# Kernel tuning notes

Measured on AMD Instinct MI355X. Metric: run time of the kernel, lower is better.

The kernel has to match this reference:

```python
import jax, jax.numpy as jnp
import numpy as np

B, T, D, H = 2, 2048, 1024, 16
HD = D // H            # 64
FH = 2752              # SwiGLU hidden: round64(int(2*4*D/3))
BETA_INIT = 0.5


def rmsnorm(x, w, eps=1e-6):
    x32 = x.astype(jnp.float32)
    r = jax.lax.rsqrt(jnp.mean(x32 * x32, axis=-1, keepdims=True) + eps)
    return (x32 * r).astype(x.dtype) * w


def rope(x, cos, sin):
    # x: (B,H,T,HD); cos/sin: (T,HD//2)
    d2 = x.shape[-1] // 2
    x1, x2 = x[..., :d2], x[..., d2:]
    return jnp.concatenate([x1 * cos - x2 * sin, x2 * cos + x1 * sin], axis=-1)


def delta_res(x, h, gn_w, g_w, g_b, wv_w, eps_k=1e-6):
    # k-hat = normalize(h); k = k_hat / sqrt(d)
    h32 = h.astype(jnp.float32)
    nrm = jnp.sqrt(jnp.sum(h32 * h32, axis=-1, keepdims=True))
    k = (h32 / jnp.maximum(nrm, eps_k)).astype(x.dtype) * (1.0 / np.sqrt(D))
    c = rmsnorm(x, gn_w)
    logit = c @ g_w + g_b                                   # (B,T)
    beta = (2.0 * jax.nn.sigmoid(logit.astype(jnp.float32))).astype(x.dtype)[..., None]
    v = jax.nn.sigmoid(x @ wv_w)[..., None]                 # (B,T,1)
    kTx = jnp.sum(k * x, axis=-1, keepdims=True)
    return x + beta * (v - kTx) * k


def setup_inputs() -> dict:
    key = jax.random.key(0)
    ks = jax.random.split(key, 12)
    s = 0.02
    gb = np.float32(np.log(BETA_INIT / 2.0 / (1.0 - BETA_INIT / 2.0 + 1e-8)))
    return {
        "x": jax.random.normal(ks[0], (B, T, D), jnp.float32),
        "wq": jax.random.normal(ks[1], (D, D), jnp.float32) * s,
        "wk": jax.random.normal(ks[2], (D, D), jnp.float32) * s,
        "wv": jax.random.normal(ks[3], (D, D), jnp.float32) * s,
        "wo": jax.random.normal(ks[4], (D, D), jnp.float32) * s,
        "qn_w": jnp.ones((HD,), jnp.float32),
        "kn_w": jnp.ones((HD,), jnp.float32),
        "attn_norm_w": jnp.ones((D,), jnp.float32),
        "g1_norm_w": jnp.ones((D,), jnp.float32),
        "g1_w": jax.random.normal(ks[5], (D,), jnp.float32) * s,
        "g1_b": jnp.asarray(gb),
        "wv1": jax.random.normal(ks[6], (D,), jnp.float32) * s,
        "mlp_norm_w": jnp.ones((D,), jnp.float32),
        "w1": jax.random.normal(ks[7], (FH, D), jnp.float32) * s,
        "w2": jax.random.normal(ks[8], (D, FH), jnp.float32) * s,
        "w3": jax.random.normal(ks[9], (FH, D), jnp.float32) * s,
        "g2_norm_w": jnp.ones((D,), jnp.float32),
        "g2_w": jax.random.normal(ks[10], (D,), jnp.float32) * s,
        "g2_b": jnp.asarray(gb),
        "wv2": jax.random.normal(ks[11], (D,), jnp.float32) * s,
    }


def reference(x, wq, wk, wv, wo, qn_w, kn_w, attn_norm_w,
              g1_norm_w, g1_w, g1_b, wv1, mlp_norm_w, w1, w2, w3,
              g2_norm_w, g2_w, g2_b, wv2):
    # ---- attention sublayer (pre-norm) ----
    xc = rmsnorm(x, attn_norm_w)
    q = (xc @ wq.T).reshape(B, T, H, HD).swapaxes(1, 2)   # (B,H,T,HD)
    k = (xc @ wk.T).reshape(B, T, H, HD).swapaxes(1, 2)
    v = (xc @ wv.T).reshape(B, T, H, HD).swapaxes(1, 2)
    q = rmsnorm(q, qn_w)
    k = rmsnorm(k, kn_w)
    inv_freq = 1.0 / (10000.0 ** (jnp.arange(0, HD, 2, dtype=jnp.float32) / HD))
    freqs = jnp.arange(T, dtype=jnp.float32)[:, None] * inv_freq[None, :]  # (T,HD/2)
    cos, sin = jnp.cos(freqs), jnp.sin(freqs)
    q = rope(q, cos, sin)
    k = rope(k, cos, sin)
    scale = 1.0 / np.sqrt(HD)
    scores = jnp.einsum('bhqd,bhkd->bhqk', q, k) * scale
    causal = jnp.where(jnp.arange(T)[:, None] >= jnp.arange(T)[None, :], 0.0, -jnp.inf).astype(scores.dtype)
    attn = jax.nn.softmax(scores + causal, axis=-1)
    out = jnp.einsum('bhqk,bhkd->bhqd', attn, v)
    h_attn = out.swapaxes(1, 2).reshape(B, T, D) @ wo.T
    x = delta_res(x, h_attn, g1_norm_w, g1_w, g1_b, wv1)
    # ---- MLP sublayer (pre-norm SwiGLU) ----
    xm = rmsnorm(x, mlp_norm_w)
    h_mlp = (jax.nn.silu(xm @ w1.T) * (xm @ w3.T)) @ w2.T
    x = delta_res(x, h_mlp, g2_norm_w, g2_w, g2_b, wv2)
    return x
```

## Files before the change

kernel.cpp:

```cpp
#include <hip/hip_runtime.h>
#include <hip/hip_bf16.h>
#include <math.h>

using bf16 = __hip_bfloat16;
typedef __bf16 bf16x8 __attribute__((ext_vector_type(8)));
typedef float f32x4 __attribute__((ext_vector_type(4)));

static constexpr int B_ = 2, T_ = 2048, D_ = 1024, H_ = 16, HD_ = 64, FH_ = 2752;
static constexpr int BT = B_ * T_;

struct __align__(8)  bh4 { bf16 h[4]; };
struct __align__(16) bh8 { bf16 h[8]; };

#define DEV static __device__ __forceinline__

DEV float b2f(bf16 v) { return __bfloat162float(v); }
DEV bf16  f2b(float v) { return __float2bfloat16(v); }
DEV __bf16 f2bb(float f) { __hip_bfloat16 h = __float2bfloat16(f); return *reinterpret_cast<__bf16*>(&h); }
DEV float sigmoidf_(float x) { return 1.0f / (1.0f + __expf(-x)); }

DEV void load4f(const bf16* p, float* v) {
    bh4 t = *reinterpret_cast<const bh4*>(p);
#pragma unroll
    for (int i = 0; i < 4; ++i) v[i] = b2f(t.h[i]);
}
DEV void load4f(const float* p, float* v) {
    float4 t = *reinterpret_cast<const float4*>(p);
    v[0] = t.x; v[1] = t.y; v[2] = t.z; v[3] = t.w;
}
DEV void store4(float* p, const float* v) {
    float4 t; t.x = v[0]; t.y = v[1]; t.z = v[2]; t.w = v[3];
    *reinterpret_cast<float4*>(p) = t;
}
DEV float waveReduceSum(float v) {
#pragma unroll
    for (int m = 32; m; m >>= 1) v += __shfl_xor(v, m);
    return v;
}

DEV void gl_lds16(const bf16* g, bf16* lds_base) {
    __builtin_amdgcn_global_load_lds(
        (const __attribute__((address_space(1))) void*)g,
        (__attribute__((address_space(3))) void*)lds_base, 16, 0, 0);
}

__global__ __launch_bounds__(256) void k_rope_tables(float* __restrict__ cost, float* __restrict__ sint) {
    int idx = blockIdx.x * 256 + threadIdx.x;
    if (idx >= T_ * 32) return;
    int t = idx >> 5, j = idx & 31;
    float inv = powf(10000.0f, -(float)j * (1.0f / 32.0f));
    float f = (float)t * inv;
    cost[idx] = cosf(f);
    sint[idx] = sinf(f);
}

__global__ __launch_bounds__(256) void k_f2b(const float* __restrict__ in, bf16* __restrict__ out, int n8) {
    int i = blockIdx.x * 256 + threadIdx.x;
    if (i >= n8) return;
    const float4* p = reinterpret_cast<const float4*>(in + (size_t)i * 8);
    float4 a = p[0], b = p[1];
    bh8 o;
    o.h[0] = f2b(a.x); o.h[1] = f2b(a.y); o.h[2] = f2b(a.z); o.h[3] = f2b(a.w);
    o.h[4] = f2b(b.x); o.h[5] = f2b(b.y); o.h[6] = f2b(b.z); o.h[7] = f2b(b.w);
    *reinterpret_cast<bh8*>(out + (size_t)i * 8) = o;
}

__global__ __launch_bounds__(256) void k_f2b_pair(const float* __restrict__ w1, const float* __restrict__ w3,
                                                  bf16* __restrict__ outp, int n8tot) {
    int i = blockIdx.x * 256 + threadIdx.x;
    if (i >= n8tot) return;
    int r = i >> 7, c8 = i & 127;
    int sel = (r >> 4) & 1;
    int j = ((r >> 5) << 4) | (r & 15);
    const float* src = (sel ? w3 : w1) + (size_t)j * D_ + c8 * 8;
    float4 a = reinterpret_cast<const float4*>(src)[0];
    float4 b = reinterpret_cast<const float4*>(src)[1];
    bh8 o;
    o.h[0] = f2b(a.x); o.h[1] = f2b(a.y); o.h[2] = f2b(a.z); o.h[3] = f2b(a.w);
    o.h[4] = f2b(b.x); o.h[5] = f2b(b.y); o.h[6] = f2b(b.z); o.h[7] = f2b(b.w);
    *reinterpret_cast<bh8*>(outp + (size_t)r * D_ + c8 * 8) = o;
}

__global__ __launch_bounds__(256) void k_rmsnorm(const float* __restrict__ x, const float* __restrict__ w,
                                                 bf16* __restrict__ out) {
    int row = blockIdx.x, tid = threadIdx.x;
    const float* xr = x + (size_t)row * D_;
    int base = tid * 4;
    float v[4];
    load4f(xr + base, v);
    float ss = v[0]*v[0] + v[1]*v[1] + v[2]*v[2] + v[3]*v[3];
    ss = waveReduceSum(ss);
    __shared__ float red[4];
    if ((tid & 63) == 0) red[tid >> 6] = ss;
    __syncthreads();
    ss = red[0] + red[1] + red[2] + red[3];
    float r = rsqrtf(ss * (1.0f / D_) + 1e-6f);
    float wv[4];
    load4f(w + base, wv);
    bh4 o;
#pragma unroll
    for (int i = 0; i < 4; ++i) o.h[i] = f2b(v[i] * r * wv[i]);
    *reinterpret_cast<bh4*>(out + (size_t)row * D_ + base) = o;
}

template <int EPI>
__global__ __launch_bounds__(512) void k_gemm256(const bf16* __restrict__ A, const bf16* __restrict__ W,
                                                 bf16* __restrict__ C, int M, int N, int K) {
    __shared__ bf16 sA[2][256 * 32];
    __shared__ bf16 sB[2][128 * 32];
    int tid = threadIdx.x, lane = tid & 63, wid = tid >> 6;
    int m0 = blockIdx.x * 256, n0 = blockIdx.y * 128;
    int wr = wid >> 1, wc = wid & 1;
    int l16 = lane & 15, lg = lane >> 4;
    int srow = lane >> 2;
    int scol = ((lane & 3) ^ ((lane >> 3) & 3)) * 8;
    int rchunk = (lg ^ ((l16 >> 1) & 3)) * 8;

    f32x4 acc[4][4] = {};

#define STAGE(buf, k0)                                                                   \
    {                                                                                    \
        _Pragma("unroll")                                                                \
        for (int c = 0; c < 2; ++c) {                                                    \
            int r0 = wid * 32 + c * 16;                                                  \
            gl_lds16(&A[(size_t)(m0 + r0 + srow) * K + (k0) + scol], &sA[buf][r0 * 32]); \
        }                                                                                \
        {                                                                                \
            int r0 = wid * 16;                                                           \
            gl_lds16(&W[(size_t)(n0 + r0 + srow) * K + (k0) + scol], &sB[buf][r0 * 32]); \
        }                                                                                \
    }

    int nk = K >> 5;
    STAGE(0, 0);
    if (nk > 1) STAGE(1, 32);
    for (int t = 0; t < nk; ++t) {
        if (t + 1 < nk) { asm volatile("s_waitcnt vmcnt(3)" ::: "memory"); }
        else            { asm volatile("s_waitcnt vmcnt(0)" ::: "memory"); }
        __builtin_amdgcn_s_barrier();
        __builtin_amdgcn_sched_barrier(0);
        int cur = t & 1;
        bf16x8 af[4], bfr[4];
#pragma unroll
        for (int m = 0; m < 4; ++m)
            af[m] = *reinterpret_cast<const bf16x8*>(&sA[cur][(wr * 64 + m * 16 + l16) * 32 + rchunk]);
#pragma unroll
        for (int n = 0; n < 4; ++n)
            bfr[n] = *reinterpret_cast<const bf16x8*>(&sB[cur][(wc * 64 + n * 16 + l16) * 32 + rchunk]);
#pragma unroll
        for (int m = 0; m < 4; ++m)
#pragma unroll
            for (int n = 0; n < 4; ++n)
                acc[m][n] = __builtin_amdgcn_mfma_f32_16x16x32_bf16(af[m], bfr[n], acc[m][n], 0, 0, 0);
        __builtin_amdgcn_sched_barrier(0);
        __builtin_amdgcn_s_barrier();
        if (t + 2 < nk) STAGE(cur, (t + 2) * 32);
    }
#undef STAGE

    int rbase = m0 + wr * 64;
    if (EPI == 1) {
        int Ng = N >> 1;
        int gbase = (n0 >> 1) + wc * 32;
#pragma unroll
        for (int m = 0; m < 4; ++m) {
#pragma unroll
            for (int n2 = 0; n2 < 2; ++n2) {
                int gcol = gbase + n2 * 16 + l16;
#pragma unroll
                for (int r = 0; r < 4; ++r) {
                    int row = rbase + m * 16 + lg * 4 + r;
                    float a1 = acc[m][n2 * 2][r];
                    float a3 = acc[m][n2 * 2 + 1][r];
                    C[(size_t)row * Ng + gcol] = f2b(a1 * sigmoidf_(a1) * a3);
                }
            }
        }
    } else {
        int cbase = n0 + wc * 64;
#pragma unroll
        for (int m = 0; m < 4; ++m) {
#pragma unroll
            for (int n = 0; n < 4; ++n) {
                int col = cbase + n * 16 + l16;
#pragma unroll
                for (int r = 0; r < 4; ++r) {
                    int row = rbase + m * 16 + lg * 4 + r;
                    C[(size_t)row * N + col] = f2b(acc[m][n][r]);
                }
            }
        }
    }
}

__global__ __launch_bounds__(256) void k_gemm64(const bf16* __restrict__ A, const bf16* __restrict__ W,
                                                bf16* __restrict__ C, int M, int N, int K) {
    __shared__ bf16 sA[2][128 * 32];
    __shared__ bf16 sB[2][64 * 32];
    int tid = threadIdx.x, lane = tid & 63, wid = tid >> 6;
    int m0 = blockIdx.x * 128, n0 = blockIdx.y * 64;
    int wr = wid;
    int l16 = lane & 15, lg = lane >> 4;
    int srow = lane >> 2;
    int scol = ((lane & 3) ^ ((lane >> 3) & 3)) * 8;
    int rchunk = (lg ^ ((l16 >> 1) & 3)) * 8;

    f32x4 acc[2][4] = {};

#define STAGE(buf, k0)                                                                   \
    {                                                                                    \
        _Pragma("unroll")                                                                \
        for (int c = 0; c < 2; ++c) {                                                    \
            int r0 = wid * 32 + c * 16;                                                  \
            gl_lds16(&A[(size_t)(m0 + r0 + srow) * K + (k0) + scol], &sA[buf][r0 * 32]); \
        }                                                                                \
        {                                                                                \
            int r0 = wid * 16;                                                           \
            gl_lds16(&W[(size_t)(n0 + r0 + srow) * K + (k0) + scol], &sB[buf][r0 * 32]); \
        }                                                                                \
    }

    int nk = K >> 5;
    STAGE(0, 0);
    if (nk > 1) STAGE(1, 32);
    for (int t = 0; t < nk; ++t) {
        if (t + 1 < nk) { asm volatile("s_waitcnt vmcnt(3)" ::: "memory"); }
        else            { asm volatile("s_waitcnt vmcnt(0)" ::: "memory"); }
        __builtin_amdgcn_s_barrier();
        __builtin_amdgcn_sched_barrier(0);
        int cur = t & 1;
        bf16x8 af[2], bfr[4];
#pragma unroll
        for (int m = 0; m < 2; ++m)
            af[m] = *reinterpret_cast<const bf16x8*>(&sA[cur][(wr * 32 + m * 16 + l16) * 32 + rchunk]);
#pragma unroll
        for (int n = 0; n < 4; ++n)
            bfr[n] = *reinterpret_cast<const bf16x8*>(&sB[cur][(n * 16 + l16) * 32 + rchunk]);
#pragma unroll
        for (int m = 0; m < 2; ++m)
#pragma unroll
            for (int n = 0; n < 4; ++n)
                acc[m][n] = __builtin_amdgcn_mfma_f32_16x16x32_bf16(af[m], bfr[n], acc[m][n], 0, 0, 0);
        __builtin_amdgcn_sched_barrier(0);
        __builtin_amdgcn_s_barrier();
        if (t + 2 < nk) STAGE(cur, (t + 2) * 32);
    }
#undef STAGE

    int rbase = m0 + wr * 32;
#pragma unroll
    for (int m = 0; m < 2; ++m) {
#pragma unroll
        for (int n = 0; n < 4; ++n) {
            int col = n0 + n * 16 + l16;
#pragma unroll
            for (int r = 0; r < 4; ++r) {
                int row = rbase + m * 16 + lg * 4 + r;
                C[(size_t)row * N + col] = f2b(acc[m][n][r]);
            }
        }
    }
}

__global__ __launch_bounds__(256) void k_qk_norm_rope(const bf16* __restrict__ qin, const float* __restrict__ wn,
                                                      const float* __restrict__ cost, const float* __restrict__ sint,
                                                      bf16* __restrict__ qout, float scale, int ld, int off) {
    int tid = threadIdx.x;
    int g = blockIdx.x * 4 + (tid >> 6);
    int d = tid & 63;
    int h = g % H_, t = (g / H_) % T_, b = g / (H_ * T_);
    float v = b2f(qin[(size_t)(b * T_ + t) * ld + off + h * HD_ + d]);
    float ss = waveReduceSum(v * v);
    float r = rsqrtf(ss * (1.0f / HD_) + 1e-6f);
    float xn = v * r * wn[d];
    float p = __shfl_xor(xn, 32);
    float c = cost[t * 32 + (d & 31)], s = sint[t * 32 + (d & 31)];
    float o = (d < 32) ? (xn * c - p * s) : (xn * c + p * s);
    qout[((size_t)(b * H_ + h) * T_ + t) * HD_ + d] = f2b(o * scale);
}

__global__ __launch_bounds__(256) void k_v_transpose(const bf16* __restrict__ vin, bf16* __restrict__ vt,
                                                     int ld, int off) {
    __shared__ bf16 tile[64][72];
    int tid = threadIdx.x;
    int bh = blockIdx.y;
    int t0 = blockIdx.x * 64;
    int b = bh >> 4, h = bh & 15;
#pragma unroll
    for (int i = 0; i < 16; ++i) {
        int lin = i * 256 + tid;
        int tl = lin >> 6, d = lin & 63;
        tile[tl][d] = vin[(size_t)(b * T_ + t0 + tl) * ld + off + h * HD_ + d];
    }
    __syncthreads();
#pragma unroll
    for (int i = 0; i < 16; ++i) {
        int lin = i * 256 + tid;
        int d = lin >> 6, tl = lin & 63;
        vt[((size_t)bh * HD_ + d) * T_ + t0 + tl] = tile[tl][d];
    }
}

template <bool MASKED>
DEV void fa3_tile(const bf16* __restrict__ kl, const bf16* __restrict__ vl,
                  int l16, int lg, int qloc,
                  const bf16x8 qf0, const bf16x8 qf1,
                  f32x4* acc, float& m_r, float& l_r) {
    f32x4 s[8];
#pragma unroll
    for (int n = 0; n < 8; ++n) {
        int kv = n * 16 + l16;
        bf16x8 kf0 = *reinterpret_cast<const bf16x8*>(&kl[kv * 64 + (((lg ^ kv) & 7) << 3)]);
        bf16x8 kf1 = *reinterpret_cast<const bf16x8*>(&kl[kv * 64 + ((((4 + lg) ^ kv) & 7) << 3)]);
        f32x4 t = {};
        t = __builtin_amdgcn_mfma_f32_16x16x32_bf16(kf0, qf0, t, 0, 0, 0);
        t = __builtin_amdgcn_mfma_f32_16x16x32_bf16(kf1, qf1, t, 0, 0, 0);
        s[n] = t;
    }
    if (MASKED) {
#pragma unroll
        for (int n = 0; n < 8; ++n)
#pragma unroll
            for (int r = 0; r < 4; ++r)
                if (n * 16 + lg * 4 + r > qloc) s[n][r] = -INFINITY;
    }
    float mx = -INFINITY;
#pragma unroll
    for (int n = 0; n < 8; ++n)
#pragma unroll
        for (int r = 0; r < 4; ++r) mx = fmaxf(mx, s[n][r]);
    mx = fmaxf(mx, __shfl_xor(mx, 16));
    mx = fmaxf(mx, __shfl_xor(mx, 32));
    float mnew = fmaxf(m_r, mx);
    float corr = __expf(m_r - mnew);
    m_r = mnew;
    float ps = 0.0f;
#pragma unroll
    for (int n = 0; n < 8; ++n)
#pragma unroll
        for (int r = 0; r < 4; ++r) {
            float e = __expf(s[n][r] - mnew);
            s[n][r] = e;
            ps += e;
        }
    l_r = l_r * corr + ps;
#pragma unroll
    for (int np = 0; np < 4; ++np) acc[np] = acc[np] * corr;

    bf16x8 pb[4];
#pragma unroll
    for (int n2 = 0; n2 < 4; ++n2)
#pragma unroll
        for (int j = 0; j < 8; ++j)
            pb[n2][j] = f2bb(s[2 * n2 + (j >> 2)][j & 3]);

    int d15 = l16;
    int eoff = (lg & 1) * 4;
#pragma unroll
    for (int n2 = 0; n2 < 4; ++n2) {
        int c0 = (n2 * 4 + (lg >> 1));
        int c1 = c0 + 2;
#pragma unroll
        for (int np = 0; np < 4; ++np) {
            int d = np * 16 + l16;
            union { bf16x8 v; bh4 q[2]; } u;
            u.q[0] = *reinterpret_cast<const bh4*>(&vl[d * 128 + ((c0 ^ d15) << 3) + eoff]);
            u.q[1] = *reinterpret_cast<const bh4*>(&vl[d * 128 + ((c1 ^ d15) << 3) + eoff]);
            acc[np] = __builtin_amdgcn_mfma_f32_16x16x32_bf16(u.v, pb[n2], acc[np], 0, 0, 0);
        }
    }
}

__global__ __launch_bounds__(256) void k_flash(const bf16* __restrict__ Q, const bf16* __restrict__ Kk,
                                               const bf16* __restrict__ Vt, bf16* __restrict__ Out) {
    __shared__ bf16 kl[128 * 64];
    __shared__ bf16 vl[64 * 128];
    int tid = threadIdx.x, lane = tid & 63, w = tid >> 6;
    int l16 = lane & 15, lg = lane >> 4;
    int L = blockIdx.x;
    int xcd = L & 7, m = L >> 3;
    int bh = xcd * 4 + (m & 3);
    int qi = (T_ / 128 - 1) - (m >> 2);
    int q0 = qi * 128;
    int b = bh >> 4, h = bh & 15;
    const bf16* qb = Q + (size_t)bh * T_ * HD_;
    const bf16* kb = Kk + (size_t)bh * T_ * HD_;
    const bf16* vb = Vt + (size_t)bh * HD_ * T_;

    bf16x8 qfr[2][2];
#pragma unroll
    for (int f = 0; f < 2; ++f) {
        int qrow = q0 + w * 32 + f * 16 + l16;
        const bf16* qp = qb + (size_t)qrow * HD_ + lg * 8;
        qfr[f][0] = *reinterpret_cast<const bf16x8*>(qp);
        qfr[f][1] = *reinterpret_cast<const bf16x8*>(qp + 32);
    }
    f32x4 acc[2][4] = {};
    float m_r[2] = {-INFINITY, -INFINITY};
    float l_r[2] = {0.0f, 0.0f};

    for (int kv0 = 0; kv0 <= q0; kv0 += 128) {
        __syncthreads();
#pragma unroll
        for (int i = 0; i < 4; ++i) {
            int idx = i * 256 + tid;
            int kv = idx >> 3, c = idx & 7;
            *reinterpret_cast<bh8*>(&kl[kv * 64 + (((c ^ kv) & 7) << 3)]) =
                *reinterpret_cast<const bh8*>(&kb[(size_t)(kv0 + kv) * HD_ + c * 8]);
        }
#pragma unroll
        for (int i = 0; i < 4; ++i) {
            int idx = i * 256 + tid;
            int d = idx >> 4, c = idx & 15;
            *reinterpret_cast<bh8*>(&vl[d * 128 + (((c ^ d) & 15) << 3)]) =
                *reinterpret_cast<const bh8*>(&vb[(size_t)d * T_ + kv0 + c * 8]);
        }
        __syncthreads();
        if (kv0 == q0) {
#pragma unroll
            for (int f = 0; f < 2; ++f)
                fa3_tile<true>(kl, vl, l16, lg, w * 32 + f * 16 + l16,
                               qfr[f][0], qfr[f][1], acc[f], m_r[f], l_r[f]);
        } else {
#pragma unroll
            for (int f = 0; f < 2; ++f)
                fa3_tile<false>(kl, vl, l16, lg, 0,
                                qfr[f][0], qfr[f][1], acc[f], m_r[f], l_r[f]);
        }
    }
#pragma unroll
    for (int f = 0; f < 2; ++f) {
        float lt = l_r[f];
        lt += __shfl_xor(lt, 16);
        lt += __shfl_xor(lt, 32);
        float inv = 1.0f / lt;
        int qrow = q0 + w * 32 + f * 16 + l16;
#pragma unroll
        for (int np = 0; np < 4; ++np) {
            bh4 o;
#pragma unroll
            for (int r = 0; r < 4; ++r) o.h[r] = f2b(acc[f][np][r] * inv);
            *reinterpret_cast<bh4*>(&Out[(size_t)(b * T_ + qrow) * D_ + h * HD_ + np * 16 + lg * 4]) = o;
        }
    }
}

template <int WRITE_XM>
__global__ __launch_bounds__(256) void k_delta_res(const float* __restrict__ x, const bf16* __restrict__ h,
                                                   const float* __restrict__ gn_w, const float* __restrict__ g_w,
                                                   const float* __restrict__ g_b, const float* __restrict__ wv_w,
                                                   float* __restrict__ out,
                                                   bf16* __restrict__ xm_out, const float* __restrict__ mlp_w) {
    int row = blockIdx.x, tid = threadIdx.x;
    int base = tid * 4;
    float xv[4], hv[4], gnv[4], gwv[4], wvv[4];
    load4f(x + (size_t)row * D_ + base, xv);
    load4f(h + (size_t)row * D_ + base, hv);
    load4f(gn_w + base, gnv);
    load4f(g_w + base, gwv);
    load4f(wv_w + base, wvv);
    float s_h2 = 0, s_x2 = 0, s_xg = 0, s_xv = 0, s_hx = 0;
#pragma unroll
    for (int i = 0; i < 4; ++i) {
        s_h2 += hv[i] * hv[i];
        s_x2 += xv[i] * xv[i];
        s_xg += xv[i] * gnv[i] * gwv[i];
        s_xv += xv[i] * wvv[i];
        s_hx += hv[i] * xv[i];
    }
    s_h2 = waveReduceSum(s_h2); s_x2 = waveReduceSum(s_x2); s_xg = waveReduceSum(s_xg);
    s_xv = waveReduceSum(s_xv); s_hx = waveReduceSum(s_hx);
    __shared__ float red[4][5];
    int wid = tid >> 6;
    if ((tid & 63) == 0) {
        red[wid][0] = s_h2; red[wid][1] = s_x2; red[wid][2] = s_xg;
        red[wid][3] = s_xv; red[wid][4] = s_hx;
    }
    __syncthreads();
    s_h2 = red[0][0] + red[1][0] + red[2][0] + red[3][0];
    s_x2 = red[0][1] + red[1][1] + red[2][1] + red[3][1];
    s_xg = red[0][2] + red[1][2] + red[2][2] + red[3][2];
    s_xv = red[0][3] + red[1][3] + red[2][3] + red[3][3];
    s_hx = red[0][4] + red[1][4] + red[2][4] + red[3][4];

    float r = rsqrtf(s_x2 * (1.0f / D_) + 1e-6f);
    float logit = r * s_xg + g_b[0];
    float beta = 2.0f * sigmoidf_(logit);
    float vsig = sigmoidf_(s_xv);
    float nrm = sqrtf(s_h2);
    float ks = (1.0f / 32.0f) / fmaxf(nrm, 1e-6f);
    float coef = beta * (vsig - ks * s_hx) * ks;
    float o[4];
#pragma unroll
    for (int i = 0; i < 4; ++i) o[i] = xv[i] + coef * hv[i];
    store4(out + (size_t)row * D_ + base, o);

    if (WRITE_XM) {
        float s2 = o[0]*o[0] + o[1]*o[1] + o[2]*o[2] + o[3]*o[3];
        s2 = waveReduceSum(s2);
        __shared__ float red2[4];
        __syncthreads();
        if ((tid & 63) == 0) red2[wid] = s2;
        __syncthreads();
        s2 = red2[0] + red2[1] + red2[2] + red2[3];
        float rr = rsqrtf(s2 * (1.0f / D_) + 1e-6f);
        float mw[4];
        load4f(mlp_w + base, mw);
        bh4 ob;
#pragma unroll
        for (int i = 0; i < 4; ++i) ob.h[i] = f2b(o[i] * rr * mw[i]);
        *reinterpret_cast<bh4*>(xm_out + (size_t)row * D_ + base) = ob;
    }
}

extern "C" void kernel_launch(void* const* d_in, const int* in_sizes, int n_in,
                              void* d_out, int out_size, void* d_ws, size_t ws_size,
                              hipStream_t stream) {
    const float* x       = (const float*)d_in[0];
    const float* wq      = (const float*)d_in[1];
    const float* wk      = (const float*)d_in[2];
    const float* wv      = (const float*)d_in[3];
    const float* wo      = (const float*)d_in[4];
    const float* qn_w    = (const float*)d_in[5];
    const float* kn_w    = (const float*)d_in[6];
    const float* attn_nw = (const float*)d_in[7];
    const float* g1_nw   = (const float*)d_in[8];
    const float* g1_w    = (const float*)d_in[9];
    const float* g1_b    = (const float*)d_in[10];
    const float* wv1     = (const float*)d_in[11];
    const float* mlp_nw  = (const float*)d_in[12];
    const float* w1      = (const float*)d_in[13];
    const float* w2      = (const float*)d_in[14];
    const float* w3      = (const float*)d_in[15];
    const float* g2_nw   = (const float*)d_in[16];
    const float* g2_w    = (const float*)d_in[17];
    const float* g2_b    = (const float*)d_in[18];
    const float* wv2     = (const float*)d_in[19];
    float* out = (float*)d_out;

    char* ws = (char*)d_ws;
    const size_t KB = 1024;
    const size_t MB = 1024 * 1024;
    float* cost = (float*)(ws);
    float* sint = (float*)(ws + 256 * KB);
    bf16* XC = (bf16*)(ws + 512 * KB);
    bf16* Bb = (bf16*)(ws + 512 * KB + 8  * MB);
    bf16* Cb = (bf16*)(ws + 512 * KB + 16 * MB);
    bf16* Db = (bf16*)(ws + 512 * KB + 24 * MB);
    bf16* Eb = (bf16*)(ws + 512 * KB + 32 * MB);
    bf16* Fb = (bf16*)(ws + 512 * KB + 40 * MB);
    bf16* Gb = (bf16*)(ws + 512 * KB + 48 * MB);
    float* x1 = (float*)(ws + 512 * KB + 56 * MB);

    bf16* wqkv = Eb;
    bf16* qkv  = Bb;
    bf16* wbo  = XC;
    bf16* attn_out = Bb;
    bf16* wpair = Bb;
    bf16* w2b  = Db;
    bf16* g    = Eb;
    bf16* hmlp = XC;

    const int nDD = D_ * D_ / 8, nFD = FH_ * D_ / 8;
    dim3 blk(256);

    k_rope_tables<<<dim3((T_ * 32) / 256), blk, 0, stream>>>(cost, sint);

    k_rmsnorm<<<dim3(BT), blk, 0, stream>>>(x, attn_nw, XC);
    k_f2b<<<dim3((nDD + 255) / 256), blk, 0, stream>>>(wq, wqkv, nDD);
    k_f2b<<<dim3((nDD + 255) / 256), blk, 0, stream>>>(wk, wqkv + (size_t)D_ * D_, nDD);
    k_f2b<<<dim3((nDD + 255) / 256), blk, 0, stream>>>(wv, wqkv + (size_t)2 * D_ * D_, nDD);

    k_gemm256<0><<<dim3(16, 24), dim3(512), 0, stream>>>(XC, wqkv, qkv, BT, 3 * D_, D_);

    k_qk_norm_rope<<<dim3(BT * H_ / 4), blk, 0, stream>>>(qkv, qn_w, cost, sint, Eb, 0.125f, 3 * D_, 0);
    k_qk_norm_rope<<<dim3(BT * H_ / 4), blk, 0, stream>>>(qkv, kn_w, cost, sint, Fb, 1.0f, 3 * D_, D_);
    k_v_transpose<<<dim3(T_ / 64, B_ * H_), blk, 0, stream>>>(qkv, Gb, 3 * D_, 2 * D_);

    k_f2b<<<dim3((nDD + 255) / 256), blk, 0, stream>>>(wo, wbo, nDD);
    k_flash<<<dim3((T_ / 128) * B_ * H_), blk, 0, stream>>>(Eb, Fb, Gb, attn_out);

    k_gemm64<<<dim3(32, 16), blk, 0, stream>>>(attn_out, wbo, Cb, BT, D_, D_);

    k_delta_res<1><<<dim3(BT), blk, 0, stream>>>(x, Cb, g1_nw, g1_w, g1_b, wv1, x1, XC, mlp_nw);

    k_f2b_pair<<<dim3((2 * nFD + 255) / 256), blk, 0, stream>>>(w1, w3, wpair, 2 * nFD);
    k_f2b<<<dim3((nFD + 255) / 256), blk, 0, stream>>>(w2, w2b, nFD);

    k_gemm256<1><<<dim3(16, 43), dim3(512), 0, stream>>>(XC, wpair, g, BT, 2 * FH_, D_);

    k_gemm64<<<dim3(32, 16), blk, 0, stream>>>(g, w2b, hmlp, BT, D_, FH_);

    k_delta_res<0><<<dim3(BT), blk, 0, stream>>>(x1, hmlp, g2_nw, g2_w, g2_b, wv2, out, nullptr, nullptr);
}
```

Before: 282.9 us.

## Load GEMM A-fragments directly from global into registers, dropping A shared-memory staging

Both GEMM kernels stop staging the A tile through LDS. Each wave now loads its own A fragments straight from global memory into registers, double-buffered in two register sets, and only the shared W tile still goes through LDS. The loop is unrolled by two with adjusted vmcnt waits. This removes LDS traffic and LDS capacity for A, which could allow higher occupancy. The cost is more registers, uncoalesced per-row global loads, and duplicate A reads across the two column waves. Launch-bounds occupancy hints are also added to the GEMM and flash kernels.

```diff
diff --git a/kernel.cpp b/kernel.cpp
--- a/kernel.cpp
+++ b/kernel.cpp
@@ -104,9 +104,8 @@
 }
 
 template <int EPI>
-__global__ __launch_bounds__(512) void k_gemm256(const bf16* __restrict__ A, const bf16* __restrict__ W,
-                                                 bf16* __restrict__ C, int M, int N, int K) {
-    __shared__ bf16 sA[2][256 * 32];
+__global__ __launch_bounds__(512, 3) void k_gemm256(const bf16* __restrict__ A, const bf16* __restrict__ W,
+                                                    bf16* __restrict__ C, int M, int N, int K) {
     __shared__ bf16 sB[2][128 * 32];
     int tid = threadIdx.x, lane = tid & 63, wid = tid >> 6;
     int m0 = blockIdx.x * 256, n0 = blockIdx.y * 128;
@@ -116,47 +115,58 @@
     int scol = ((lane & 3) ^ ((lane >> 3) & 3)) * 8;
     int rchunk = (lg ^ ((l16 >> 1) & 3)) * 8;
 
+    const bf16* Ab = A + (size_t)(m0 + wr * 64 + l16) * K + lg * 8;
+
     f32x4 acc[4][4] = {};
-
-#define STAGE(buf, k0)                                                                   \
+    bf16x8 afA[4], afB[4];
+
+#define STB(buf, k0)                                                                     \
+    {                                                                                    \
+        int r0 = wid * 16;                                                               \
+        gl_lds16(&W[(size_t)(n0 + r0 + srow) * K + (k0) + scol], &sB[buf][r0 * 32]);     \
+    }
+#define GLA(dst, k0)                                                                     \
     {                                                                                    \
         _Pragma("unroll")                                                                \
-        for (int c = 0; c < 2; ++c) {                                                    \
-            int r0 = wid * 32 + c * 16;                                                  \
-            gl_lds16(&A[(size_t)(m0 + r0 + srow) * K + (k0) + scol], &sA[buf][r0 * 32]); \
-        }                                                                                \
-        {                                                                                \
-            int r0 = wid * 16;                                                           \
-            gl_lds16(&W[(size_t)(n0 + r0 + srow) * K + (k0) + scol], &sB[buf][r0 * 32]); \
-        }                                                                                \
+        for (int m = 0; m < 4; ++m)                                                      \
+            dst[m] = *reinterpret_cast<const bf16x8*>(Ab + (size_t)m * 16 * K + (k0));   \
+    }
+#define COMPUTE(buf, af)                                                                 \
+    {                                                                                    \
+        bf16x8 bfr[4];                                                                   \
+        _Pragma("unroll")                                                                \
+        for (int n = 0; n < 4; ++n)                                                      \
+            bfr[n] = *reinterpret_cast<const bf16x8*>(&sB[buf][(wc * 64 + n * 16 + l16) * 32 + rchunk]); \
+        _Pragma("unroll")                                                                \
+        for (int m = 0; m < 4; ++m)                                                      \
+            _Pragma("unroll")                                                            \
+            for (int n = 0; n < 4; ++n)                                                  \
+                acc[m][n] = __builtin_amdgcn_mfma_f32_16x16x32_bf16(af[m], bfr[n], acc[m][n], 0, 0, 0); \
     }
 
     int nk = K >> 5;
-    STAGE(0, 0);
-    if (nk > 1) STAGE(1, 32);
-    for (int t = 0; t < nk; ++t) {
-        if (t + 1 < nk) { asm volatile("s_waitcnt vmcnt(3)" ::: "memory"); }
+    STB(0, 0); GLA(afA, 0);
+    STB(1, 32); GLA(afB, 32);
+    for (int t = 0; t < nk; t += 2) {
+        asm volatile("s_waitcnt vmcnt(5)" ::: "memory");
+        __builtin_amdgcn_s_barrier();
+        __builtin_amdgcn_sched_barrier(0);
+        COMPUTE(0, afA);
+        __builtin_amdgcn_sched_barrier(0);
+        __builtin_amdgcn_s_barrier();
+        if (t + 2 < nk) { STB(0, (t + 2) * 32); GLA(afA, (t + 2) * 32); }
+        if (t + 2 < nk) { asm volatile("s_waitcnt vmcnt(5)" ::: "memory"); }
         else            { asm volatile("s_waitcnt vmcnt(0)" ::: "memory"); }
         __builtin_amdgcn_s_barrier();
         __builtin_amdgcn_sched_barrier(0);
-        int cur = t & 1;
-        bf16x8 af[4], bfr[4];
-#pragma unroll
-        for (int m = 0; m < 4; ++m)
-            af[m] = *reinterpret_cast<const bf16x8*>(&sA[cur][(wr * 64 + m * 16 + l16) * 32 + rchunk]);
-#pragma unroll
-        for (int n = 0; n < 4; ++n)
-            bfr[n] = *reinterpret_cast<const bf16x8*>(&sB[cur][(wc * 64 + n * 16 + l16) * 32 + rchunk]);
-#pragma unroll
-        for (int m = 0; m < 4; ++m)
-#pragma unroll
-            for (int n = 0; n < 4; ++n)
-                acc[m][n] = __builtin_amdgcn_mfma_f32_16x16x32_bf16(af[m], bfr[n], acc[m][n], 0, 0, 0);
-        __builtin_amdgcn_sched_barrier(0);
-        __builtin_amdgcn_s_barrier();
-        if (t + 2 < nk) STAGE(cur, (t + 2) * 32);
-    }
-#undef STAGE
+        COMPUTE(1, afB);
+        __builtin_amdgcn_sched_barrier(0);
+        __builtin_amdgcn_s_barrier();
+        if (t + 3 < nk) { STB(1, (t + 3) * 32); GLA(afB, (t + 3) * 32); }
+    }
+#undef STB
+#undef GLA
+#undef COMPUTE
 
     int rbase = m0 + wr * 64;
     if (EPI == 1) {
@@ -193,61 +203,70 @@
     }
 }
 
-__global__ __launch_bounds__(256) void k_gemm64(const bf16* __restrict__ A, const bf16* __restrict__ W,
-                                                bf16* __restrict__ C, int M, int N, int K) {
-    __shared__ bf16 sA[2][128 * 32];
+__global__ __launch_bounds__(256, 4) void k_gemm64(const bf16* __restrict__ A, const bf16* __restrict__ W,
+                                                   bf16* __restrict__ C, int M, int N, int K) {
     __shared__ bf16 sB[2][64 * 32];
     int tid = threadIdx.x, lane = tid & 63, wid = tid >> 6;
     int m0 = blockIdx.x * 128, n0 = blockIdx.y * 64;
-    int wr = wid;
     int l16 = lane & 15, lg = lane >> 4;
     int srow = lane >> 2;
     int scol = ((lane & 3) ^ ((lane >> 3) & 3)) * 8;
     int rchunk = (lg ^ ((l16 >> 1) & 3)) * 8;
 
+    const bf16* Ab = A + (size_t)(m0 + wid * 32 + l16) * K + lg * 8;
+
     f32x4 acc[2][4] = {};
-
-#define STAGE(buf, k0)                                                                   \
+    bf16x8 afA[2], afB[2];
+
+#define STB(buf, k0)                                                                     \
+    {                                                                                    \
+        int r0 = wid * 16;                                                               \
+        gl_lds16(&W[(size_t)(n0 + r0 + srow) * K + (k0) + scol], &sB[buf][r0 * 32]);     \
+    }
+#define GLA(dst, k0)                                                                     \
     {                                                                                    \
         _Pragma("unroll")                                                                \
-        for (int c = 0; c < 2; ++c) {                                                    \
-            int r0 = wid * 32 + c * 16;                                                  \
-            gl_lds16(&A[(size_t)(m0 + r0 + srow) * K + (k0) + scol], &sA[buf][r0 * 32]); \
-        }                                                                                \
-        {                                                                                \
-            int r0 = wid * 16;                                                           \
-            gl_lds16(&W[(size_t)(n0 + r0 + srow) * K + (k0) + scol], &sB[buf][r0 * 32]); \
-        }                                                                                \
+        for (int m = 0; m < 2; ++m)                                                      \
+            dst[m] = *reinterpret_cast<const bf16x8*>(Ab + (size_t)m * 16 * K + (k0));   \
+    }
+#define COMPUTE(buf, af)                                                                 \
+    {                                                                                    \
+        bf16x8 bfr[4];                                                                   \
+        _Pragma("unroll")                                                                \
+        for (int n = 0; n < 4; ++n)                                                      \
+            bfr[n] = *reinterpret_cast<const bf16x8*>(&sB[buf][(n * 16 + l16) * 32 + rchunk]); \
+        _Pragma("unroll")                                                                \
+        for (int m = 0; m < 2; ++m)                                                      \
+            _Pragma("unroll")                                                            \
+            for (int n = 0; n < 4; ++n)                                                  \
+                acc[m][n] = __builtin_amdgcn_mfma_f32_16x16x32_bf16(af[m], bfr[n], acc[m][n], 0, 0, 0); \
     }
 
     int nk = K >> 5;
-    STAGE(0, 0);
-    if (nk > 1) STAGE(1, 32);
-    for (int t = 0; t < nk; ++t) {
-        if (t + 1 < nk) { asm volatile("s_waitcnt vmcnt(3)" ::: "memory"); }
+    STB(0, 0); GLA(afA, 0);
+    STB(1, 32); GLA(afB, 32);
+    for (int t = 0; t < nk; t += 2) {
+        asm volatile("s_waitcnt vmcnt(3)" ::: "memory");
+        __builtin_amdgcn_s_barrier();
+        __builtin_amdgcn_sched_barrier(0);
+        COMPUTE(0, afA);
+        __builtin_amdgcn_sched_barrier(0);
+        __builtin_amdgcn_s_barrier();
+        if (t + 2 < nk) { STB(0, (t + 2) * 32); GLA(afA, (t + 2) * 32); }
+        if (t + 2 < nk) { asm volatile("s_waitcnt vmcnt(3)" ::: "memory"); }
         else            { asm volatile("s_waitcnt vmcnt(0)" ::: "memory"); }
         __builtin_amdgcn_s_barrier();
         __builtin_amdgcn_sched_barrier(0);
-        int cur = t & 1;
-        bf16x8 af[2], bfr[4];
-#pragma unroll
-        for (int m = 0; m < 2; ++m)
-            af[m] = *reinterpret_cast<const bf16x8*>(&sA[cur][(wr * 32 + m * 16 + l16) * 32 + rchunk]);
-#pragma unroll
-        for (int n = 0; n < 4; ++n)
-            bfr[n] = *reinterpret_cast<const bf16x8*>(&sB[cur][(n * 16 + l16) * 32 + rchunk]);
-#pragma unroll
-        for (int m = 0; m < 2; ++m)
-#pragma unroll
-            for (int n = 0; n < 4; ++n)
-                acc[m][n] = __builtin_amdgcn_mfma_f32_16x16x32_bf16(af[m], bfr[n], acc[m][n], 0, 0, 0);
-        __builtin_amdgcn_sched_barrier(0);
-        __builtin_amdgcn_s_barrier();
-        if (t + 2 < nk) STAGE(cur, (t + 2) * 32);
-    }
-#undef STAGE
-
-    int rbase = m0 + wr * 32;
+        COMPUTE(1, afB);
+        __builtin_amdgcn_sched_barrier(0);
+        __builtin_amdgcn_s_barrier();
+        if (t + 3 < nk) { STB(1, (t + 3) * 32); GLA(afB, (t + 3) * 32); }
+    }
+#undef STB
+#undef GLA
+#undef COMPUTE
+
+    int rbase = m0 + wid * 32;
 #pragma unroll
     for (int m = 0; m < 2; ++m) {
 #pragma unroll
@@ -371,8 +390,8 @@
     }
 }
 
-__global__ __launch_bounds__(256) void k_flash(const bf16* __restrict__ Q, const bf16* __restrict__ Kk,
-                                               const bf16* __restrict__ Vt, bf16* __restrict__ Out) {
+__global__ __launch_bounds__(256, 3) void k_flash(const bf16* __restrict__ Q, const bf16* __restrict__ Kk,
+                                                  const bf16* __restrict__ Vt, bf16* __restrict__ Out) {
     __shared__ bf16 kl[128 * 64];
     __shared__ bf16 vl[64 * 128];
     int tid = threadIdx.x, lane = tid & 63, w = tid >> 6;
```

New measurement: 611.4 us. 116% more time.
